# Kernel tuning notes

Hardware: AMD Instinct MI355X
Metric: run time of the kernel (lower is better)

Reference implementation:

```python
import jax, jax.numpy as jnp
import numpy as np
import math

B, T, C = 2, 2048, 2048
NH, L = 16, 128  # n_head, LCompression


def setup_inputs() -> dict:
    key = jax.random.key(0)
    ks = jax.random.split(key, 7)
    s = 0.02
    return {
        "x": jax.random.normal(ks[0], (B, T, C), dtype=jnp.float32),
        # latent: Linear(n_embd -> LComp), stored as [in, out]
        "W_lat": jax.random.normal(ks[1], (C, L), dtype=jnp.float32) * s,
        "b_lat": jnp.zeros((L,), dtype=jnp.float32),
        # Wd: Linear(n_embd -> n_head*LComp)
        "W_d": jax.random.normal(ks[2], (C, NH * L), dtype=jnp.float32) * s,
        "b_d": jnp.zeros((NH * L,), dtype=jnp.float32),
        # c_proj: Linear(n_head*LComp -> n_embd)
        "W_proj": jax.random.normal(ks[3], (NH * L, C), dtype=jnp.float32) * s,
        "b_proj": jnp.zeros((C,), dtype=jnp.float32),
    }


def reference(x, W_lat, b_lat, W_d, b_d, W_proj, b_proj):
    Bx, Tx, Cx = x.shape
    # shared low-rank latent, used as both K and V (identical across heads)
    k = x @ W_lat + b_lat                                   # [B,T,L]
    q = (x @ W_d + b_d).reshape(Bx, Tx, NH, L)              # [B,T,H,L]
    q = jnp.transpose(q, (0, 2, 1, 3))                      # [B,H,T,L]
    scale = 1.0 / math.sqrt(L)
    # scores against the head-shared latent (no per-head K expansion)
    att = jnp.einsum("bhtl,bsl->bhts", q, k) * scale        # [B,H,T,T]
    causal = jnp.tril(jnp.ones((Tx, Tx), dtype=bool))
    att = jnp.where(causal[None, None], att, -jnp.inf)
    att = jax.nn.softmax(att, axis=-1)
    y = jnp.einsum("bhts,bsl->bhtl", att, k)                # [B,H,T,L]
    y = jnp.transpose(y, (0, 2, 1, 3)).reshape(Bx, Tx, NH * L)
    return y @ W_proj + b_proj                              # [B,T,C]
```

## Files before the change

kernel.cpp:

```cpp
#include <hip/hip_runtime.h>
#include <hip/hip_bf16.h>

#define B_   2
#define T_   2048
#define C_   2048
#define NH_  16
#define L_   128
#define NKQ  2176
#define MTOK 4096
#define SCALE_ 0.08838834764831845f
#define SCALE2_ 0.12753785792696073f

typedef short short8 __attribute__((ext_vector_type(8)));
typedef float f32x4  __attribute__((ext_vector_type(4)));

#define GLD16(gp, lp) __builtin_amdgcn_global_load_lds(                      \
    (const __attribute__((address_space(1))) void*)(gp),                     \
    (__attribute__((address_space(3))) void*)(lp), 16, 0, 0)

__device__ __forceinline__ unsigned short f2bf(float f) {
  union { float f; unsigned u; } x; x.f = f;
  unsigned r = x.u + 0x7fffu + ((x.u >> 16) & 1u);
  return (unsigned short)(r >> 16);
}

__global__ __launch_bounds__(256) void prep_all(
    const float* __restrict__ x, const float* __restrict__ W_lat,
    const float* __restrict__ W_d, const float* __restrict__ W_proj,
    const float* __restrict__ b_lat, const float* __restrict__ b_d,
    unsigned short* __restrict__ x_bf, unsigned short* __restrict__ BtCat,
    unsigned short* __restrict__ WprojT, float* __restrict__ biascat) {
  __shared__ float tile[32][33];
  int bid = blockIdx.x;
  const int tid = threadIdx.x;

  if (bid < 8192) {
    int i = bid * 1024 + tid * 4;
    float4 v = *(const float4*)(x + i);
    ushort4 o;
    o.x = f2bf(v.x); o.y = f2bf(v.y); o.z = f2bf(v.z); o.w = f2bf(v.w);
    *(ushort4*)(x_bf + i) = o;
    return;
  }
  bid -= 8192;

  const float* W; unsigned short* Wt; int K, N; float mul; int nbx;
  if (bid < 256) {
    W = W_lat; Wt = BtCat; K = C_; N = L_; mul = 1.f; nbx = 4;
  } else if (bid < 256 + 4096) {
    bid -= 256;
    W = W_d; Wt = BtCat + (size_t)L_ * C_; K = C_; N = NH_ * L_; mul = SCALE2_; nbx = 64;
  } else if (bid < 256 + 8192) {
    bid -= 256 + 4096;
    W = W_proj; Wt = WprojT; K = NH_ * L_; N = C_; mul = 1.f; nbx = 64;
  } else {
    int i = (bid - (256 + 8192)) * 256 + tid;
    if (i < L_) biascat[i] = b_lat[i];
    else if (i < NKQ) biascat[i] = b_d[i - L_] * SCALE2_;
    return;
  }

  const int bx = (bid % nbx) * 32, by = (bid / nbx) * 32;
  const int tx = tid & 31, ty = tid >> 5;
  #pragma unroll
  for (int i2 = 0; i2 < 4; i2++)
    tile[ty + i2 * 8][tx] = W[(size_t)(by + ty + i2 * 8) * N + bx + tx];
  __syncthreads();
  #pragma unroll
  for (int i2 = 0; i2 < 4; i2++)
    Wt[(size_t)(bx + ty + i2 * 8) * K + by + tx] = f2bf(tile[tx][ty + i2 * 8] * mul);
}

__global__ void transpose_lat(const unsigned short* __restrict__ kq,
                              unsigned short* __restrict__ KlT) {
  __shared__ unsigned short tile[32][33];
  int t0 = blockIdx.x * 32, l0 = blockIdx.y * 32, b = blockIdx.z;
  int tx = threadIdx.x, ty = threadIdx.y;
  #pragma unroll
  for (int i = 0; i < 4; i++)
    tile[ty + i * 8][tx] = kq[((size_t)b * T_ + t0 + ty + i * 8) * NKQ + l0 + tx];
  __syncthreads();
  #pragma unroll
  for (int i = 0; i < 4; i++)
    KlT[((size_t)b * L_ + l0 + ty + i * 8) * T_ + t0 + tx] = tile[tx][ty + i * 8];
}

__global__ __launch_bounds__(256) void gemm_bt_bias(
    const unsigned short* __restrict__ A,
    const unsigned short* __restrict__ Bt,
    const float* __restrict__ bias,
    unsigned short* __restrict__ Cb,
    float* __restrict__ Cf,
    int M, int N, int K) {
  __shared__ __align__(16) unsigned short As[2][128 * 32];
  __shared__ __align__(16) unsigned short Bs[2][128 * 32];
  const int tid  = threadIdx.x;
  const int wave = tid >> 6, lane = tid & 63;
  const int lcol = lane & 15, quad = lane >> 4;
  const int m0 = blockIdx.x * 128, n0 = blockIdx.y * 128;
  const int wm = (wave >> 1) * 64, wn = (wave & 1) * 64;
  const int lrow = lane >> 2, lchunk = (lane & 3) * 8;
  const int rb = wave * 32;

  f32x4 acc[4][4];
  #pragma unroll
  for (int i = 0; i < 4; i++)
    #pragma unroll
    for (int j = 0; j < 4; j++) acc[i][j] = (f32x4){0.f, 0.f, 0.f, 0.f};

  const int nk = K >> 5;
  GLD16(&A [(size_t)(m0 + rb      + lrow) * K + lchunk], &As[0][ rb       * 32]);
  GLD16(&A [(size_t)(m0 + rb + 16 + lrow) * K + lchunk], &As[0][(rb + 16) * 32]);
  GLD16(&Bt[(size_t)(n0 + rb      + lrow) * K + lchunk], &Bs[0][ rb       * 32]);
  GLD16(&Bt[(size_t)(n0 + rb + 16 + lrow) * K + lchunk], &Bs[0][(rb + 16) * 32]);

  for (int kt = 0; kt < nk; ++kt) {
    const int cur = kt & 1;
    __syncthreads();

    if (kt + 1 < nk) {
      const int kc = (kt + 1) << 5;
      GLD16(&A [(size_t)(m0 + rb      + lrow) * K + kc + lchunk], &As[cur ^ 1][ rb       * 32]);
      GLD16(&A [(size_t)(m0 + rb + 16 + lrow) * K + kc + lchunk], &As[cur ^ 1][(rb + 16) * 32]);
      GLD16(&Bt[(size_t)(n0 + rb      + lrow) * K + kc + lchunk], &Bs[cur ^ 1][ rb       * 32]);
      GLD16(&Bt[(size_t)(n0 + rb + 16 + lrow) * K + kc + lchunk], &Bs[cur ^ 1][(rb + 16) * 32]);
    }

    short8 af[4], bfr[4];
    #pragma unroll
    for (int i = 0; i < 4; i++)
      af[i] = *(const short8*)&As[cur][(wm + i * 16 + lcol) * 32 + quad * 8];
    #pragma unroll
    for (int j = 0; j < 4; j++)
      bfr[j] = *(const short8*)&Bs[cur][(wn + j * 16 + lcol) * 32 + quad * 8];
    #pragma unroll
    for (int i = 0; i < 4; i++)
      #pragma unroll
      for (int j = 0; j < 4; j++)
        acc[i][j] = __builtin_amdgcn_mfma_f32_16x16x32_bf16(af[i], bfr[j], acc[i][j], 0, 0, 0);
  }

  #pragma unroll
  for (int i = 0; i < 4; i++) {
    #pragma unroll
    for (int j = 0; j < 4; j++) {
      int col = n0 + wn + j * 16 + lcol;
      float bv = bias[col];
      #pragma unroll
      for (int r = 0; r < 4; r++) {
        int row = m0 + wm + i * 16 + quad * 4 + r;
        float v = acc[i][j][r] + bv;
        if (Cf) Cf[(size_t)row * N + col] = v;
        else    Cb[(size_t)row * N + col] = f2bf(v);
      }
    }
  }
}

__global__ __launch_bounds__(256, 2) void attn_mla(
    const unsigned short* __restrict__ kq,
    const unsigned short* __restrict__ KlT,
    unsigned short* __restrict__ y) {
  __shared__ __align__(16) unsigned short Kr[2][64 * 128];
  __shared__ __align__(16) unsigned short Kt[2][128 * 64];
  __shared__ __align__(16) unsigned short Pls[4][32 * 64];

  const int tid  = threadIdx.x;
  const int wave = tid >> 6, lane = tid & 63;
  const int lcol = lane & 15, quad = lane >> 4;
  const int n    = blockIdx.x;
  const int slot = n >> 8, c = n & 255;
  const int hg   = c >> 5, qi = c & 31;
  const int b    = hg >> 2;
  const int h    = (hg & 3) * 4 + wave;
  const int qt32 = slot ? qi : (63 - qi);
  const size_t rowbase = (size_t)b * T_;
  const int q0 = qt32 * 32;
  unsigned short* Pw = &Pls[wave][0];

  short8 qf[2][4];
  #pragma unroll
  for (int i = 0; i < 2; i++) {
    const unsigned short* qp = kq + (rowbase + q0 + i * 16 + lcol) * NKQ + L_ + h * L_;
    #pragma unroll
    for (int kc = 0; kc < 4; kc++)
      qf[i][kc] = *(const short8*)(qp + kc * 32 + quad * 8);
  }

  f32x4 acco[2][8];
  #pragma unroll
  for (int i = 0; i < 2; i++)
    #pragma unroll
    for (int ns = 0; ns < 8; ns++) acco[i][ns] = (f32x4){0.f, 0.f, 0.f, 0.f};
  float lsum[2][4];
  #pragma unroll
  for (int i = 0; i < 2; i++)
    #pragma unroll
    for (int r = 0; r < 4; r++) lsum[i][r] = 0.f;

  const int nt = (qt32 >> 1) + 1;

  #pragma unroll
  for (int kk = 0; kk < 4; kk++) {
    int r0 = wave * 16 + kk * 4;
    int rg = r0 + (lane >> 4);
    int cl = ((lane & 15) ^ (rg & 7)) * 8;
    GLD16(kq + (rowbase + rg) * NKQ + cl, &Kr[0][r0 * 128]);
  }
  #pragma unroll
  for (int kk = 0; kk < 4; kk++) {
    int r0 = wave * 32 + kk * 8;
    int rg = r0 + (lane >> 3);
    int cl = ((lane & 7) ^ (rg & 7)) * 8;
    GLD16(KlT + ((size_t)b * L_ + rg) * T_ + cl, &Kt[0][r0 * 64]);
  }

  for (int ts = 0; ts < nt; ts++) {
    const int cur = ts & 1;
    __syncthreads();

    if (ts + 1 < nt) {
      const int s1 = (ts + 1) * 64;
      #pragma unroll
      for (int kk = 0; kk < 4; kk++) {
        int r0 = wave * 16 + kk * 4;
        int rg = r0 + (lane >> 4);
        int cl = ((lane & 15) ^ (rg & 7)) * 8;
        GLD16(kq + (rowbase + s1 + rg) * NKQ + cl, &Kr[cur ^ 1][r0 * 128]);
      }
      #pragma unroll
      for (int kk = 0; kk < 4; kk++) {
        int r0 = wave * 32 + kk * 8;
        int rg = r0 + (lane >> 3);
        int cl = ((lane & 7) ^ (rg & 7)) * 8;
        GLD16(KlT + ((size_t)b * L_ + rg) * T_ + s1 + cl, &Kt[cur ^ 1][r0 * 64]);
      }
    }

    const unsigned short* Krc = &Kr[cur][0];
    const unsigned short* Ktc = &Kt[cur][0];

    f32x4 accs[2][4];
    #pragma unroll
    for (int i = 0; i < 2; i++)
      #pragma unroll
      for (int ns = 0; ns < 4; ns++) accs[i][ns] = (f32x4){0.f, 0.f, 0.f, 0.f};
    __builtin_amdgcn_s_setprio(1);
    #pragma unroll
    for (int kc = 0; kc < 4; kc++)
      #pragma unroll
      for (int ns = 0; ns < 4; ns++) {
        short8 bfrag = *(const short8*)&Krc[(ns * 16 + lcol) * 128 +
                                            (((kc * 4 + quad) ^ (lcol & 7)) * 8)];
        #pragma unroll
        for (int i = 0; i < 2; i++)
          accs[i][ns] = __builtin_amdgcn_mfma_f32_16x16x32_bf16(qf[i][kc], bfrag, accs[i][ns], 0, 0, 0);
      }
    __builtin_amdgcn_s_setprio(0);

    const bool diag = (ts == nt - 1);
    #pragma unroll
    for (int half = 0; half < 2; half++) {
      #pragma unroll
      for (int i = 0; i < 2; i++)
        #pragma unroll
        for (int n2 = 0; n2 < 2; n2++) {
          const int ns = half * 2 + n2;
          #pragma unroll
          for (int r = 0; r < 4; r++) {
            float v = accs[i][ns][r];
            int sg = ns * 16 + lcol;
            int qg = (qt32 & 1) * 32 + i * 16 + quad * 4 + r;
            if (diag && sg > qg) v = -1e30f;
            float e = __builtin_amdgcn_exp2f(v);
            unsigned eu = __float_as_uint(e) & 0xffff0000u;
            lsum[i][r] += __uint_as_float(eu);
            int row = i * 16 + quad * 4 + r;
            int col = ns * 16 + lcol;
            int phys = ((col >> 3) ^ (row & 7));
            Pw[row * 64 + phys * 8 + (col & 7)] = (unsigned short)(eu >> 16);
          }
        }

      short8 pa[2];
      #pragma unroll
      for (int i = 0; i < 2; i++)
        pa[i] = *(const short8*)&Pw[(i * 16 + lcol) * 64 +
                                    (((half * 4 + quad) ^ (lcol & 7)) * 8)];
      __builtin_amdgcn_s_setprio(1);
      #pragma unroll
      for (int ns = 0; ns < 8; ns++) {
        short8 bfrag = *(const short8*)&Ktc[(ns * 16 + lcol) * 64 +
                                            (((half * 4 + quad) ^ (lcol & 7)) * 8)];
        #pragma unroll
        for (int i = 0; i < 2; i++)
          acco[i][ns] = __builtin_amdgcn_mfma_f32_16x16x32_bf16(pa[i], bfrag, acco[i][ns], 0, 0, 0);
      }
      __builtin_amdgcn_s_setprio(0);
    }
  }

  #pragma unroll
  for (int i = 0; i < 2; i++)
    #pragma unroll
    for (int r = 0; r < 4; r++) {
      float s = lsum[i][r];
      #pragma unroll
      for (int off = 1; off < 16; off <<= 1) s += __shfl_xor(s, off, 64);
      lsum[i][r] = 1.f / s;
    }

  #pragma unroll
  for (int i = 0; i < 2; i++)
    #pragma unroll
    for (int ns = 0; ns < 8; ns++)
      #pragma unroll
      for (int r = 0; r < 4; r++) {
        int qg = q0 + i * 16 + quad * 4 + r;
        y[(rowbase + qg) * (NH_ * L_) + h * L_ + ns * 16 + lcol] =
            f2bf(acco[i][ns][r] * lsum[i][r]);
      }
}

extern "C" void kernel_launch(void* const* d_in, const int* in_sizes, int n_in,
                              void* d_out, int out_size, void* d_ws, size_t ws_size,
                              hipStream_t stream) {
  const float* x      = (const float*)d_in[0];
  const float* W_lat  = (const float*)d_in[1];
  const float* b_lat  = (const float*)d_in[2];
  const float* W_d    = (const float*)d_in[3];
  const float* b_d    = (const float*)d_in[4];
  const float* W_proj = (const float*)d_in[5];
  const float* b_proj = (const float*)d_in[6];
  float* out = (float*)d_out;

  unsigned short* x_bf   = (unsigned short*)d_ws;
  unsigned short* BtCat  = x_bf   + (size_t)MTOK * C_;
  unsigned short* WprojT = BtCat  + (size_t)NKQ * C_;
  unsigned short* kqbuf  = WprojT + (size_t)C_ * (NH_ * L_);
  unsigned short* ybuf   = kqbuf  + (size_t)MTOK * NKQ;
  unsigned short* KlT    = ybuf   + (size_t)MTOK * (NH_ * L_);
  float*          biascat = (float*)(KlT + (size_t)B_ * L_ * T_);

  prep_all<<<16649, 256, 0, stream>>>(x, W_lat, W_d, W_proj, b_lat, b_d,
                                      x_bf, BtCat, WprojT, biascat);
  gemm_bt_bias<<<dim3(MTOK / 128, NKQ / 128), 256, 0, stream>>>(
      x_bf, BtCat, biascat, kqbuf, nullptr, MTOK, NKQ, C_);
  transpose_lat<<<dim3(T_ / 32, L_ / 32, B_), dim3(32, 8), 0, stream>>>(kqbuf, KlT);
  attn_mla<<<512, 256, 0, stream>>>(kqbuf, KlT, ybuf);
  gemm_bt_bias<<<dim3(MTOK / 128, C_ / 128), 256, 0, stream>>>(
      ybuf, WprojT, b_proj, nullptr, out, MTOK, C_, C_);
}
```

Measured before the change: 282.5 us.

## Switch attention to 32x32x16 MFMA with transposed scores and register-resident P

The attention kernel moves from 16x16x32 to 32x32x16 bf16 MFMA. It computes S^T (K as the A operand, Q as B) so the exponentiated scores can be packed to bf16 with v_cvt_pk_bf16_f32 and rearranged with v_permlane32_swap directly into the A-operand layout of the PV MFMA. This removes the per-wave LDS round trip for P. The LDS swizzles for K and K^T are widened to match the new access patterns, and the row-sum normalisation goes through a small LDS buffer plus one block barrier at the end. The aim is fewer LDS writes and reads and fewer MFMA issues, at the cost of larger accumulator register tiles that could raise register pressure.

```diff
diff --git a/kernel.cpp b/kernel.cpp
--- a/kernel.cpp
+++ b/kernel.cpp
@@ -8,11 +8,11 @@
 #define L_   128
 #define NKQ  2176
 #define MTOK 4096
-#define SCALE_ 0.08838834764831845f
 #define SCALE2_ 0.12753785792696073f
 
 typedef short short8 __attribute__((ext_vector_type(8)));
 typedef float f32x4  __attribute__((ext_vector_type(4)));
+typedef float f32x16 __attribute__((ext_vector_type(16)));
 
 #define GLD16(gp, lp) __builtin_amdgcn_global_load_lds(                      \
     (const __attribute__((address_space(1))) void*)(gp),                     \
@@ -163,11 +163,11 @@
     unsigned short* __restrict__ y) {
   __shared__ __align__(16) unsigned short Kr[2][64 * 128];
   __shared__ __align__(16) unsigned short Kt[2][128 * 64];
-  __shared__ __align__(16) unsigned short Pls[4][32 * 64];
+  __shared__ __align__(16) float ls[4][32];
 
   const int tid  = threadIdx.x;
   const int wave = tid >> 6, lane = tid & 63;
-  const int lcol = lane & 15, quad = lane >> 4;
+  const int l31 = lane & 31, hf = lane >> 5;
   const int n    = blockIdx.x;
   const int slot = n >> 8, c = n & 255;
   const int hg   = c >> 5, qi = c & 31;
@@ -176,27 +176,22 @@
   const int qt32 = slot ? qi : (63 - qi);
   const size_t rowbase = (size_t)b * T_;
   const int q0 = qt32 * 32;
-  unsigned short* Pw = &Pls[wave][0];
-
-  short8 qf[2][4];
-  #pragma unroll
-  for (int i = 0; i < 2; i++) {
-    const unsigned short* qp = kq + (rowbase + q0 + i * 16 + lcol) * NKQ + L_ + h * L_;
-    #pragma unroll
-    for (int kc = 0; kc < 4; kc++)
-      qf[i][kc] = *(const short8*)(qp + kc * 32 + quad * 8);
-  }
-
-  f32x4 acco[2][8];
-  #pragma unroll
-  for (int i = 0; i < 2; i++)
-    #pragma unroll
-    for (int ns = 0; ns < 8; ns++) acco[i][ns] = (f32x4){0.f, 0.f, 0.f, 0.f};
-  float lsum[2][4];
-  #pragma unroll
-  for (int i = 0; i < 2; i++)
-    #pragma unroll
-    for (int r = 0; r < 4; r++) lsum[i][r] = 0.f;
+
+  short8 qf[8];
+  {
+    const unsigned short* qp =
+        kq + (rowbase + q0 + l31) * NKQ + L_ + h * L_ + hf * 8;
+    #pragma unroll
+    for (int kc = 0; kc < 8; kc++)
+      qf[kc] = *(const short8*)(qp + kc * 16);
+  }
+
+  f32x16 acco[4];
+  #pragma unroll
+  for (int nb = 0; nb < 4; nb++)
+    #pragma unroll
+    for (int r = 0; r < 16; r++) acco[nb][r] = 0.f;
+  float lsum = 0.f;
 
   const int nt = (qt32 >> 1) + 1;
 
@@ -204,14 +199,14 @@
   for (int kk = 0; kk < 4; kk++) {
     int r0 = wave * 16 + kk * 4;
     int rg = r0 + (lane >> 4);
-    int cl = ((lane & 15) ^ (rg & 7)) * 8;
+    int cl = ((lane & 15) ^ (rg & 15)) * 8;
     GLD16(kq + (rowbase + rg) * NKQ + cl, &Kr[0][r0 * 128]);
   }
   #pragma unroll
   for (int kk = 0; kk < 4; kk++) {
     int r0 = wave * 32 + kk * 8;
     int rg = r0 + (lane >> 3);
-    int cl = ((lane & 7) ^ (rg & 7)) * 8;
+    int cl = ((lane & 7) ^ (rg & 7) ^ (((rg >> 3) & 1) << 2)) * 8;
     GLD16(KlT + ((size_t)b * L_ + rg) * T_ + cl, &Kt[0][r0 * 64]);
   }
 
@@ -225,14 +220,14 @@
       for (int kk = 0; kk < 4; kk++) {
         int r0 = wave * 16 + kk * 4;
         int rg = r0 + (lane >> 4);
-        int cl = ((lane & 15) ^ (rg & 7)) * 8;
+        int cl = ((lane & 15) ^ (rg & 15)) * 8;
         GLD16(kq + (rowbase + s1 + rg) * NKQ + cl, &Kr[cur ^ 1][r0 * 128]);
       }
       #pragma unroll
       for (int kk = 0; kk < 4; kk++) {
         int r0 = wave * 32 + kk * 8;
         int rg = r0 + (lane >> 3);
-        int cl = ((lane & 7) ^ (rg & 7)) * 8;
+        int cl = ((lane & 7) ^ (rg & 7) ^ (((rg >> 3) & 1) << 2)) * 8;
         GLD16(KlT + ((size_t)b * L_ + rg) * T_ + s1 + cl, &Kt[cur ^ 1][r0 * 64]);
       }
     }
@@ -240,86 +235,85 @@
     const unsigned short* Krc = &Kr[cur][0];
     const unsigned short* Ktc = &Kt[cur][0];
 
-    f32x4 accs[2][4];
-    #pragma unroll
-    for (int i = 0; i < 2; i++)
-      #pragma unroll
-      for (int ns = 0; ns < 4; ns++) accs[i][ns] = (f32x4){0.f, 0.f, 0.f, 0.f};
+    f32x16 accs[2];
+    #pragma unroll
+    for (int sb = 0; sb < 2; sb++)
+      #pragma unroll
+      for (int r = 0; r < 16; r++) accs[sb][r] = 0.f;
     __builtin_amdgcn_s_setprio(1);
     #pragma unroll
-    for (int kc = 0; kc < 4; kc++)
-      #pragma unroll
-      for (int ns = 0; ns < 4; ns++) {
-        short8 bfrag = *(const short8*)&Krc[(ns * 16 + lcol) * 128 +
-                                            (((kc * 4 + quad) ^ (lcol & 7)) * 8)];
-        #pragma unroll
-        for (int i = 0; i < 2; i++)
-          accs[i][ns] = __builtin_amdgcn_mfma_f32_16x16x32_bf16(qf[i][kc], bfrag, accs[i][ns], 0, 0, 0);
+    for (int kc = 0; kc < 8; kc++)
+      #pragma unroll
+      for (int sb = 0; sb < 2; sb++) {
+        short8 kf = *(const short8*)&Krc[(sb * 32 + l31) * 128 +
+                                          (((2 * kc + hf) ^ (l31 & 15)) * 8)];
+        accs[sb] = __builtin_amdgcn_mfma_f32_32x32x16_bf16(kf, qf[kc], accs[sb], 0, 0, 0);
       }
     __builtin_amdgcn_s_setprio(0);
 
     const bool diag = (ts == nt - 1);
-    #pragma unroll
-    for (int half = 0; half < 2; half++) {
-      #pragma unroll
-      for (int i = 0; i < 2; i++)
-        #pragma unroll
-        for (int n2 = 0; n2 < 2; n2++) {
-          const int ns = half * 2 + n2;
-          #pragma unroll
-          for (int r = 0; r < 4; r++) {
-            float v = accs[i][ns][r];
-            int sg = ns * 16 + lcol;
-            int qg = (qt32 & 1) * 32 + i * 16 + quad * 4 + r;
-            if (diag && sg > qg) v = -1e30f;
-            float e = __builtin_amdgcn_exp2f(v);
-            unsigned eu = __float_as_uint(e) & 0xffff0000u;
-            lsum[i][r] += __uint_as_float(eu);
-            int row = i * 16 + quad * 4 + r;
-            int col = ns * 16 + lcol;
-            int phys = ((col >> 3) ^ (row & 7));
-            Pw[row * 64 + phys * 8 + (col & 7)] = (unsigned short)(eu >> 16);
-          }
-        }
-
-      short8 pa[2];
-      #pragma unroll
-      for (int i = 0; i < 2; i++)
-        pa[i] = *(const short8*)&Pw[(i * 16 + lcol) * 64 +
-                                    (((half * 4 + quad) ^ (lcol & 7)) * 8)];
+    const int qg = (qt32 & 1) * 32 + l31;
+    #pragma unroll
+    for (int sb = 0; sb < 2; sb++)
+      #pragma unroll
+      for (int r = 0; r < 16; r++) {
+        float v = accs[sb][r];
+        int s64 = sb * 32 + (r & 3) + 8 * (r >> 2) + 4 * hf;
+        if (diag && s64 > qg) v = -1e30f;
+        accs[sb][r] = __builtin_amdgcn_exp2f(v);
+      }
+
+    #pragma unroll
+    for (int kc = 0; kc < 4; kc++) {
+      const int sb = kc >> 1;
+      const int t0 = (kc & 1) * 2;
+      unsigned w00, w01, w10, w11;
+      asm("v_cvt_pk_bf16_f32 %0, %1, %2" : "=v"(w00)
+          : "v"(accs[sb][4 * t0 + 0]), "v"(accs[sb][4 * t0 + 1]));
+      asm("v_cvt_pk_bf16_f32 %0, %1, %2" : "=v"(w01)
+          : "v"(accs[sb][4 * t0 + 2]), "v"(accs[sb][4 * t0 + 3]));
+      asm("v_cvt_pk_bf16_f32 %0, %1, %2" : "=v"(w10)
+          : "v"(accs[sb][4 * t0 + 4]), "v"(accs[sb][4 * t0 + 5]));
+      asm("v_cvt_pk_bf16_f32 %0, %1, %2" : "=v"(w11)
+          : "v"(accs[sb][4 * t0 + 6]), "v"(accs[sb][4 * t0 + 7]));
+      asm volatile("v_permlane32_swap_b32 %0, %1" : "+v"(w00), "+v"(w10));
+      asm volatile("v_permlane32_swap_b32 %0, %1" : "+v"(w01), "+v"(w11));
+      union { short8 s; unsigned u[4]; } F;
+      F.u[0] = w00; F.u[1] = w01; F.u[2] = w10; F.u[3] = w11;
+      #pragma unroll
+      for (int w = 0; w < 4; w++) {
+        lsum += __uint_as_float(F.u[w] << 16);
+        lsum += __uint_as_float(F.u[w] & 0xffff0000u);
+      }
       __builtin_amdgcn_s_setprio(1);
       #pragma unroll
-      for (int ns = 0; ns < 8; ns++) {
-        short8 bfrag = *(const short8*)&Ktc[(ns * 16 + lcol) * 64 +
-                                            (((half * 4 + quad) ^ (lcol & 7)) * 8)];
-        #pragma unroll
-        for (int i = 0; i < 2; i++)
-          acco[i][ns] = __builtin_amdgcn_mfma_f32_16x16x32_bf16(pa[i], bfrag, acco[i][ns], 0, 0, 0);
+      for (int nb = 0; nb < 4; nb++) {
+        int rowv = nb * 32 + l31;
+        short8 vf = *(const short8*)&Ktc[rowv * 64 +
+            (((2 * kc + hf) ^ (rowv & 7) ^ (((rowv >> 3) & 1) << 2)) * 8)];
+        acco[nb] = __builtin_amdgcn_mfma_f32_32x32x16_bf16(F.s, vf, acco[nb], 0, 0, 0);
       }
       __builtin_amdgcn_s_setprio(0);
     }
   }
 
-  #pragma unroll
-  for (int i = 0; i < 2; i++)
-    #pragma unroll
-    for (int r = 0; r < 4; r++) {
-      float s = lsum[i][r];
-      #pragma unroll
-      for (int off = 1; off < 16; off <<= 1) s += __shfl_xor(s, off, 64);
-      lsum[i][r] = 1.f / s;
-    }
-
-  #pragma unroll
-  for (int i = 0; i < 2; i++)
-    #pragma unroll
-    for (int ns = 0; ns < 8; ns++)
-      #pragma unroll
-      for (int r = 0; r < 4; r++) {
-        int qg = q0 + i * 16 + quad * 4 + r;
-        y[(rowbase + qg) * (NH_ * L_) + h * L_ + ns * 16 + lcol] =
-            f2bf(acco[i][ns][r] * lsum[i][r]);
-      }
+  lsum += __shfl_xor(lsum, 32, 64);
+  if (lane < 32) ls[wave][l31] = 1.f / lsum;
+  __syncthreads();
+  f32x4 rv[4];
+  #pragma unroll
+  for (int t = 0; t < 4; t++)
+    rv[t] = *(const f32x4*)&ls[wave][8 * t + 4 * hf];
+
+  #pragma unroll
+  for (int nb = 0; nb < 4; nb++)
+    #pragma unroll
+    for (int r = 0; r < 16; r++) {
+      int q = q0 + (r & 3) + 8 * (r >> 2) + 4 * hf;
+      int l = nb * 32 + l31;
+      y[(rowbase + q) * (NH_ * L_) + h * L_ + l] =
+          f2bf(acco[nb][r] * rv[r >> 2][r & 3]);
+    }
 }
 
 extern "C" void kernel_launch(void* const* d_in, const int* in_sizes, int n_in,
```

After: 277.5 us. About the same (-1.8%).
